# Kernel optimization log

Measured on AMD Instinct MI355X. Metric: run time of the kernel, lower is better.

## Reference

```python
import jax, jax.numpy as jnp
import numpy as np

D_MODEL = 1024
N_HEADS = 16
HEAD_DIM = D_MODEL // N_HEADS
SOFTMAX_SCALE = 1.0 / np.sqrt(HEAD_DIM).astype(np.float32)


def setup_inputs() -> dict:
    key = jax.random.key(0)
    k1, k2, k3, k4, k5 = jax.random.split(key, 5)
    B, S = 2, 2048
    bound_qkv = 1.0 / np.sqrt(D_MODEL)
    x = jax.random.normal(k1, (B, S, D_MODEL), dtype=jnp.float32)
    # torch nn.Linear stores weight as [out_features, in_features]
    Wqkv_w = jax.random.uniform(k2, (3 * D_MODEL, D_MODEL), jnp.float32, -bound_qkv, bound_qkv)
    Wqkv_b = jax.random.uniform(k3, (3 * D_MODEL,), jnp.float32, -bound_qkv, bound_qkv)
    Wout_w = jax.random.uniform(k4, (D_MODEL, D_MODEL), jnp.float32, -bound_qkv, bound_qkv)
    Wout_b = jax.random.uniform(k5, (D_MODEL,), jnp.float32, -bound_qkv, bound_qkv)
    return {"x": x, "Wqkv_w": Wqkv_w, "Wqkv_b": Wqkv_b, "Wout_w": Wout_w, "Wout_b": Wout_b}


def reference(x, Wqkv_w, Wqkv_b, Wout_w, Wout_b):
    B, S, D = x.shape
    # fused QKV projection
    qkv = jnp.einsum('bsd,ed->bse', x, Wqkv_w) + Wqkv_b  # [B, S, 3D]
    q, k, v = jnp.split(qkv, 3, axis=2)
    # b s (h d) -> b h s d
    q = q.reshape(B, S, N_HEADS, HEAD_DIM).transpose(0, 2, 1, 3)
    k = k.reshape(B, S, N_HEADS, HEAD_DIM).transpose(0, 2, 1, 3)
    v = v.reshape(B, S, N_HEADS, HEAD_DIM).transpose(0, 2, 1, 3)
    attn = jnp.einsum('bhsd,bhtd->bhst', q, k) * SOFTMAX_SCALE
    attn = jax.nn.softmax(attn, axis=-1)
    ctx = jnp.einsum('bhst,bhtd->bhsd', attn, v)
    ctx = ctx.transpose(0, 2, 1, 3).reshape(B, S, D)
    out = jnp.einsum('bsd,ed->bse', ctx, Wout_w) + Wout_b
    return out
```

## Files before the change

### kernel.cpp

```cpp
#include <hip/hip_runtime.h>
#include <hip/hip_bf16.h>

typedef __attribute__((ext_vector_type(8))) __bf16 bfrag;
typedef __attribute__((ext_vector_type(4))) float f32x4;
typedef __attribute__((ext_vector_type(16))) float f32x16;
typedef __attribute__((ext_vector_type(8))) unsigned short u16x8;
typedef __attribute__((ext_vector_type(4))) unsigned short u16x4;
typedef __attribute__((ext_vector_type(4))) unsigned int u32x4;

#define SEQ 2048
#define NH 16
#define HD 64
#define DMODEL 1024
#define MTOT 4096
#define QSCALE 0.18033688011112042f

static __device__ __forceinline__ unsigned short f2bf(float f) {
  unsigned int u = __builtin_bit_cast(unsigned int, f);
  u += 0x7FFFu + ((u >> 16) & 1u);
  return (unsigned short)(u >> 16);
}

static __device__ __forceinline__ unsigned cvt_pk_bf16(float lo, float hi) {
  unsigned r;
  asm("v_cvt_pk_bf16_f32 %0, %1, %2" : "=v"(r) : "v"(lo), "v"(hi));
  return r;
}

static __device__ __forceinline__ float rsum16(const f32x16 v) {
  float a0 = v[0] + v[1], a1 = v[2] + v[3], a2 = v[4] + v[5], a3 = v[6] + v[7];
  float a4 = v[8] + v[9], a5 = v[10] + v[11], a6 = v[12] + v[13], a7 = v[14] + v[15];
  float b0 = a0 + a1, b1 = a2 + a3, b2 = a4 + a5, b3 = a6 + a7;
  return (b0 + b1) + (b2 + b3);
}

#define XG 524288
#define WQG 393216
#define WOG 131072
__global__ __launch_bounds__(256) void cvt_all_kernel(const float* __restrict__ x,
                                                      const float* __restrict__ wq,
                                                      const float* __restrict__ wo,
                                                      unsigned short* __restrict__ out) {
  int i = blockIdx.x * 256 + threadIdx.x;
  if (i >= XG + WQG + WOG) return;
  const float4* p;
  if (i < XG) p = reinterpret_cast<const float4*>(x) + (size_t)i * 2;
  else if (i < XG + WQG) p = reinterpret_cast<const float4*>(wq) + (size_t)(i - XG) * 2;
  else p = reinterpret_cast<const float4*>(wo) + (size_t)(i - XG - WQG) * 2;
  float4 a = p[0], b = p[1];
  u16x8 o;
  o[0] = f2bf(a.x); o[1] = f2bf(a.y); o[2] = f2bf(a.z); o[3] = f2bf(a.w);
  o[4] = f2bf(b.x); o[5] = f2bf(b.y); o[6] = f2bf(b.z); o[7] = f2bf(b.w);
  *(reinterpret_cast<u16x8*>(out) + i) = o;
}

#define GLDS(gp, lp)                                                       \
  __builtin_amdgcn_global_load_lds(                                        \
      (const __attribute__((address_space(1))) void*)(gp),                 \
      (__attribute__((address_space(3))) void*)(lp), 16, 0, 0)

template <int EPI>
__global__ __launch_bounds__(256) void gemm_bt_kernel(
    const unsigned short* __restrict__ A, const unsigned short* __restrict__ B,
    const float* __restrict__ bias, unsigned short* __restrict__ q_out,
    unsigned short* __restrict__ k_out, unsigned short* __restrict__ v_out,
    float* __restrict__ f_out, int M, int N, int K) {
  __shared__ __align__(16) unsigned short As[3][4096];
  __shared__ __align__(16) unsigned short Bs[3][4096];
  const int t = threadIdx.x;
  const int l = t & 63, w = t >> 6;
  const int total = gridDim.x * gridDim.y;
  const int lid0 = blockIdx.y * gridDim.x + blockIdx.x;
  const int nl = (lid0 & 7) * (total >> 3) + (lid0 >> 3);
  const int m0 = (nl / gridDim.x) * 128, n0 = (nl % gridDim.x) * 128;
  const int wrow = (w >> 1) * 64, wcol = (w & 1) * 64;
  const int lrow = l & 15, lk = (l >> 4) * 8;
  const int srow = t >> 2;
  const int scol = ((t & 3) ^ (srow & 3)) * 8;
  f32x4 acc[4][4] = {};

#define GSTAGE(buf, K0)                                                     \
  do {                                                                      \
    GLDS(A + (size_t)(m0 + srow) * K + (K0) + scol, &As[buf][0] + t * 8);   \
    GLDS(A + (size_t)(m0 + srow + 64) * K + (K0) + scol,                    \
         &As[buf][0] + 2048 + t * 8);                                       \
    GLDS(B + (size_t)(n0 + srow) * K + (K0) + scol, &Bs[buf][0] + t * 8);   \
    GLDS(B + (size_t)(n0 + srow + 64) * K + (K0) + scol,                    \
         &Bs[buf][0] + 2048 + t * 8);                                       \
  } while (0)

  const int nsteps = K >> 5;
  GSTAGE(0, 0);
  GSTAGE(1, 32);
#pragma unroll 1
  for (int ks = 0; ks < nsteps; ++ks) {
    if (ks < nsteps - 1)
      asm volatile("s_waitcnt vmcnt(4)" ::: "memory");
    else
      asm volatile("s_waitcnt vmcnt(0)" ::: "memory");
    __builtin_amdgcn_s_barrier();
    __builtin_amdgcn_sched_barrier(0);
    if (ks + 2 < nsteps) GSTAGE((ks + 2) % 3, (ks + 2) * 32);
    const unsigned short* Ac = &As[ks % 3][0];
    const unsigned short* Bc = &Bs[ks % 3][0];
    bfrag af[4], bf[4];
#pragma unroll
    for (int mt = 0; mt < 4; ++mt) {
      int row = wrow + mt * 16 + lrow;
      af[mt] = *(const bfrag*)&Ac[row * 32 + (lk ^ ((row & 3) << 3))];
    }
#pragma unroll
    for (int nt = 0; nt < 4; ++nt) {
      int row = wcol + nt * 16 + lrow;
      bf[nt] = *(const bfrag*)&Bc[row * 32 + (lk ^ ((row & 3) << 3))];
    }
#pragma unroll
    for (int mt = 0; mt < 4; ++mt)
#pragma unroll
      for (int nt = 0; nt < 4; ++nt)
        acc[mt][nt] =
            __builtin_amdgcn_mfma_f32_16x16x32_bf16(af[mt], bf[nt], acc[mt][nt], 0, 0, 0);
  }
#undef GSTAGE
#pragma unroll
  for (int nt = 0; nt < 4; ++nt) {
    int gn = n0 + wcol + nt * 16 + lrow;
    float bv = bias[gn];
    if constexpr (EPI == 0) {
      int sel = gn >> 10;
      int e = gn & 1023;
      int h = e >> 6, d = e & 63;
#pragma unroll
      for (int mt = 0; mt < 4; ++mt) {
#pragma unroll
        for (int r = 0; r < 4; ++r) {
          int gm = m0 + wrow + mt * 16 + (l >> 4) * 4 + r;
          int b = gm >> 11, s = gm & 2047;
          float fv = acc[mt][nt][r] + bv;
          if (sel == 0)
            q_out[((size_t)(b * NH + h) * SEQ + s) * HD + d] = f2bf(fv * QSCALE);
          else if (sel == 1)
            k_out[((size_t)(b * NH + h) * SEQ + s) * HD + d] = f2bf(fv);
          else
            v_out[((size_t)(b * NH + h) * HD + d) * SEQ + s] = f2bf(fv);
        }
      }
    } else {
#pragma unroll
      for (int mt = 0; mt < 4; ++mt) {
#pragma unroll
        for (int r = 0; r < 4; ++r) {
          int gm = m0 + wrow + mt * 16 + (l >> 4) * 4 + r;
          f_out[(size_t)gm * N + gn] = acc[mt][nt][r] + bv;
        }
      }
    }
  }
}

__global__ __launch_bounds__(256, 2)
void attn_kernel(const unsigned short* __restrict__ Q,
                 const unsigned short* __restrict__ Km,
                 const unsigned short* __restrict__ Vt,
                 unsigned short* __restrict__ Ctx) {
  __shared__ __align__(16) unsigned short Ks[2][128 * 64];
  __shared__ __align__(16) unsigned short Vs[2][64 * 128];
  const int t = threadIdx.x;
  const int l = t & 63, w = t >> 6;
  const int q31 = l & 31, h = l >> 5;
  const int lid = blockIdx.y * gridDim.x + blockIdx.x;
  const int bh = (lid & 7) * 4 + ((lid >> 3) >> 4);
  const int q0 = ((lid >> 3) & 15) * 128 + w * 32;
  const unsigned short* qb = Q + (size_t)bh * SEQ * HD;
  const unsigned short* kb = Km + (size_t)bh * SEQ * HD;
  const unsigned short* vb = Vt + (size_t)bh * HD * SEQ;

  bfrag qf[4];
#pragma unroll
  for (int c = 0; c < 4; ++c)
    qf[c] = *(const bfrag*)&qb[(size_t)(q0 + q31) * HD + c * 16 + h * 8];

  f32x16 acc0 = {}, acc1 = {};
  float llocal = 0.f;

  const int skr = t >> 3;
  const int sks = ((t & 7) ^ (skr & 7)) * 8;
  const int svr = t >> 4;
  const int svs = ((t & 15) ^ svr) * 8;

#define STAGE(buf, T)                                                          \
  do {                                                                         \
    const int kv0_ = (T) * 128;                                                \
    _Pragma("unroll") for (int j = 0; j < 4; ++j)                              \
        GLDS(kb + (size_t)(kv0_ + 32 * j + skr) * HD + sks,                    \
             &Ks[buf][0] + j * 2048 + t * 8);                                  \
    _Pragma("unroll") for (int j = 0; j < 4; ++j)                              \
        GLDS(vb + (size_t)(16 * j + svr) * SEQ + kv0_ + svs,                   \
             &Vs[buf][0] + j * 2048 + t * 8);                                  \
  } while (0)

  STAGE(0, 0);
  __syncthreads();

  const int sw7 = q31 & 7, sw15 = q31 & 15;
  const int st0 = w & 3;

#define LOADK(kfv, stx)                                                        \
  _Pragma("unroll") for (int c = 0; c < 4; ++c)                                \
      kfv[c] = *(const bfrag*)&Kc[((stx) * 32 + q31) * 64 +                    \
                                  (((2 * c + h) ^ sw7) * 8)]

#define QK4(dst, kfv)                                                          \
  do {                                                                         \
    dst = (f32x16){};                                                          \
    __builtin_amdgcn_s_setprio(1);                                             \
    _Pragma("unroll") for (int c = 0; c < 4; ++c)                              \
        dst = __builtin_amdgcn_mfma_f32_32x32x16_bf16(kfv[c], qf[c], dst, 0, 0, 0); \
    __builtin_amdgcn_s_setprio(0);                                             \
  } while (0)

#define SOFTPV(stx, SV)                                                        \
  do {                                                                         \
    _Pragma("unroll") for (int r = 0; r < 16; ++r)                             \
        SV[r] = __builtin_amdgcn_exp2f(SV[r]);                                 \
    llocal += rsum16(SV);                                                      \
    _Pragma("unroll") for (int u = 0; u < 2; ++u) {                            \
      const int win = (stx) * 2 + u;                                           \
      const int bse = u * 8;                                                   \
      unsigned pk0 = cvt_pk_bf16(SV[bse + 0], SV[bse + 1]);                    \
      unsigned pk1 = cvt_pk_bf16(SV[bse + 2], SV[bse + 3]);                    \
      unsigned pk2 = cvt_pk_bf16(SV[bse + 4], SV[bse + 5]);                    \
      unsigned pk3 = cvt_pk_bf16(SV[bse + 6], SV[bse + 7]);                    \
      auto w02 = __builtin_amdgcn_permlane32_swap(pk0, pk2, false, false);     \
      auto w13 = __builtin_amdgcn_permlane32_swap(pk1, pk3, false, false);     \
      u32x4 bw = {(unsigned)w02[0], (unsigned)w13[0], (unsigned)w02[1],        \
                  (unsigned)w13[1]};                                           \
      bfrag pb = __builtin_bit_cast(bfrag, bw);                                \
      const int vchunk = ((win * 2 + h) ^ sw15) * 8;                           \
      bfrag vf0 = *(const bfrag*)&Vc[q31 * 128 + vchunk];                      \
      bfrag vf1 = *(const bfrag*)&Vc[(32 + q31) * 128 + vchunk];               \
      __builtin_amdgcn_s_setprio(1);                                           \
      acc0 = __builtin_amdgcn_mfma_f32_32x32x16_bf16(vf0, pb, acc0, 0, 0, 0);  \
      acc1 = __builtin_amdgcn_mfma_f32_32x32x16_bf16(vf1, pb, acc1, 0, 0, 0);  \
      __builtin_amdgcn_s_setprio(0);                                           \
    }                                                                          \
  } while (0)

#pragma unroll 1
  for (int t2 = 0; t2 < 16; ++t2) {
    const unsigned short* Kc = &Ks[t2 & 1][0];
    const unsigned short* Vc = &Vs[t2 & 1][0];
    bfrag kfa[4], kfb[4];
    f32x16 scur, snxt;
    LOADK(kfa, st0);
    QK4(scur, kfa);
    if (t2 < 15) STAGE((t2 + 1) & 1, t2 + 1);
#pragma unroll
    for (int j = 0; j < 4; ++j) {
      if (j < 3) {
        const int stn = (st0 + j + 1) & 3;
        LOADK(kfb, stn);
        QK4(snxt, kfb);
      }
      const int stc = (st0 + j) & 3;
      SOFTPV(stc, scur);
      scur = snxt;
    }
    __syncthreads();
  }
#undef STAGE
#undef LOADK
#undef QK4
#undef SOFTPV

  const int b = bh >> 4, head = bh & 15;
  float lsum = llocal + __shfl_xor(llocal, 32);
  const float inv = __builtin_amdgcn_rcpf(lsum);
  unsigned short* cp = Ctx + ((size_t)(b * SEQ + (q0 + q31)) * NH + head) * HD;
#pragma unroll
  for (int dt = 0; dt < 2; ++dt) {
    const f32x16 av = dt ? acc1 : acc0;
#pragma unroll
    for (int rq = 0; rq < 4; ++rq) {
      u16x4 o;
#pragma unroll
      for (int rr = 0; rr < 4; ++rr) o[rr] = f2bf(av[rq * 4 + rr] * inv);
      *(u16x4*)&cp[dt * 32 + rq * 8 + h * 4] = o;
    }
  }
}

extern "C" void kernel_launch(void* const* d_in, const int* in_sizes, int n_in,
                              void* d_out, int out_size, void* d_ws, size_t ws_size,
                              hipStream_t stream) {
  const float* x = (const float*)d_in[0];
  const float* wqkv = (const float*)d_in[1];
  const float* bqkv = (const float*)d_in[2];
  const float* wout = (const float*)d_in[3];
  const float* bout = (const float*)d_in[4];
  float* out = (float*)d_out;

  unsigned short* xb = (unsigned short*)d_ws;
  unsigned short* wqkvb = xb + (size_t)MTOT * DMODEL;
  unsigned short* woutb = wqkvb + (size_t)3 * DMODEL * DMODEL;
  unsigned short* qb = woutb + (size_t)DMODEL * DMODEL;
  unsigned short* kb = qb + (size_t)32 * SEQ * HD;
  unsigned short* vtb = kb + (size_t)32 * SEQ * HD;
  unsigned short* ctxb = vtb + (size_t)32 * SEQ * HD;

  cvt_all_kernel<<<(XG + WQG + WOG + 255) / 256, 256, 0, stream>>>(x, wqkv, wout, xb);
  gemm_bt_kernel<0><<<dim3(3 * DMODEL / 128, MTOT / 128), 256, 0, stream>>>(
      xb, wqkvb, bqkv, qb, kb, vtb, nullptr, MTOT, 3 * DMODEL, DMODEL);
  attn_kernel<<<dim3(SEQ / 128, 32), 256, 0, stream>>>(qb, kb, vtb, ctxb);
  gemm_bt_kernel<1><<<dim3(DMODEL / 128, MTOT / 128), 256, 0, stream>>>(
      ctxb, woutb, bout, nullptr, nullptr, nullptr, out, MTOT, DMODEL, DMODEL);
}
```

Baseline: 119.7 us.

## Switch GEMM to BK=64 double-buffered pipeline with 8-way XOR swizzle

The GEMM K-tile grows from 32 to 64, and the 3-stage LDS ring with fine-grained vmcnt waits becomes a 2-stage double buffer synchronised with __syncthreads. The LDS swizzle widens from 4-way to 8-way to match the 64-element rows. The aim is to halve the number of loop iterations and barriers and issue more MFMAs per step. In exchange, prefetch depth drops from two stages to one and the loop ends on a full-block barrier, which may expose more global-load latency.

```diff
diff --git a/kernel.cpp b/kernel.cpp
--- a/kernel.cpp
+++ b/kernel.cpp
@@ -65,8 +65,8 @@
     const float* __restrict__ bias, unsigned short* __restrict__ q_out,
     unsigned short* __restrict__ k_out, unsigned short* __restrict__ v_out,
     float* __restrict__ f_out, int M, int N, int K) {
-  __shared__ __align__(16) unsigned short As[3][4096];
-  __shared__ __align__(16) unsigned short Bs[3][4096];
+  __shared__ __align__(16) unsigned short As[2][8192];
+  __shared__ __align__(16) unsigned short Bs[2][8192];
   const int t = threadIdx.x;
   const int l = t & 63, w = t >> 6;
   const int total = gridDim.x * gridDim.y;
@@ -74,52 +74,53 @@
   const int nl = (lid0 & 7) * (total >> 3) + (lid0 >> 3);
   const int m0 = (nl / gridDim.x) * 128, n0 = (nl % gridDim.x) * 128;
   const int wrow = (w >> 1) * 64, wcol = (w & 1) * 64;
-  const int lrow = l & 15, lk = (l >> 4) * 8;
-  const int srow = t >> 2;
-  const int scol = ((t & 3) ^ (srow & 3)) * 8;
+  const int lrow = l & 15, hi = l >> 4;
+  const int srow = t >> 3;
+  const int scol = ((t & 7) ^ (srow & 7)) * 8;
   f32x4 acc[4][4] = {};
 
-#define GSTAGE(buf, K0)                                                     \
-  do {                                                                      \
-    GLDS(A + (size_t)(m0 + srow) * K + (K0) + scol, &As[buf][0] + t * 8);   \
-    GLDS(A + (size_t)(m0 + srow + 64) * K + (K0) + scol,                    \
-         &As[buf][0] + 2048 + t * 8);                                       \
-    GLDS(B + (size_t)(n0 + srow) * K + (K0) + scol, &Bs[buf][0] + t * 8);   \
-    GLDS(B + (size_t)(n0 + srow + 64) * K + (K0) + scol,                    \
-         &Bs[buf][0] + 2048 + t * 8);                                       \
+#define GSTAGE(buf, K0)                                                       \
+  do {                                                                        \
+    _Pragma("unroll") for (int j = 0; j < 4; ++j)                             \
+        GLDS(A + (size_t)(m0 + j * 32 + srow) * K + (K0) + scol,              \
+             &As[buf][0] + j * 2048 + t * 8);                                 \
+    _Pragma("unroll") for (int j = 0; j < 4; ++j)                             \
+        GLDS(B + (size_t)(n0 + j * 32 + srow) * K + (K0) + scol,              \
+             &Bs[buf][0] + j * 2048 + t * 8);                                 \
   } while (0)
 
-  const int nsteps = K >> 5;
+  const int nsteps = K >> 6;
   GSTAGE(0, 0);
-  GSTAGE(1, 32);
+  __syncthreads();
 #pragma unroll 1
-  for (int ks = 0; ks < nsteps; ++ks) {
-    if (ks < nsteps - 1)
-      asm volatile("s_waitcnt vmcnt(4)" ::: "memory");
-    else
-      asm volatile("s_waitcnt vmcnt(0)" ::: "memory");
-    __builtin_amdgcn_s_barrier();
-    __builtin_amdgcn_sched_barrier(0);
-    if (ks + 2 < nsteps) GSTAGE((ks + 2) % 3, (ks + 2) * 32);
-    const unsigned short* Ac = &As[ks % 3][0];
-    const unsigned short* Bc = &Bs[ks % 3][0];
-    bfrag af[4], bf[4];
+  for (int kt = 0; kt < nsteps; ++kt) {
+    if (kt < nsteps - 1) GSTAGE((kt + 1) & 1, (kt + 1) * 64);
+    const unsigned short* Ac = &As[kt & 1][0];
+    const unsigned short* Bc = &Bs[kt & 1][0];
+    bfrag af[4][2], bf[4][2];
 #pragma unroll
     for (int mt = 0; mt < 4; ++mt) {
-      int row = wrow + mt * 16 + lrow;
-      af[mt] = *(const bfrag*)&Ac[row * 32 + (lk ^ ((row & 3) << 3))];
+      const int row = wrow + mt * 16 + lrow;
+#pragma unroll
+      for (int ks = 0; ks < 2; ++ks)
+        af[mt][ks] = *(const bfrag*)&Ac[row * 64 + (((hi + ks * 4) ^ (row & 7)) * 8)];
     }
 #pragma unroll
     for (int nt = 0; nt < 4; ++nt) {
-      int row = wcol + nt * 16 + lrow;
-      bf[nt] = *(const bfrag*)&Bc[row * 32 + (lk ^ ((row & 3) << 3))];
+      const int row = wcol + nt * 16 + lrow;
+#pragma unroll
+      for (int ks = 0; ks < 2; ++ks)
+        bf[nt][ks] = *(const bfrag*)&Bc[row * 64 + (((hi + ks * 4) ^ (row & 7)) * 8)];
     }
 #pragma unroll
     for (int mt = 0; mt < 4; ++mt)
 #pragma unroll
       for (int nt = 0; nt < 4; ++nt)
-        acc[mt][nt] =
-            __builtin_amdgcn_mfma_f32_16x16x32_bf16(af[mt], bf[nt], acc[mt][nt], 0, 0, 0);
+#pragma unroll
+        for (int ks = 0; ks < 2; ++ks)
+          acc[mt][nt] = __builtin_amdgcn_mfma_f32_16x16x32_bf16(af[mt][ks], bf[nt][ks],
+                                                                acc[mt][nt], 0, 0, 0);
+    __syncthreads();
   }
 #undef GSTAGE
 #pragma unroll
@@ -134,7 +135,7 @@
       for (int mt = 0; mt < 4; ++mt) {
 #pragma unroll
         for (int r = 0; r < 4; ++r) {
-          int gm = m0 + wrow + mt * 16 + (l >> 4) * 4 + r;
+          int gm = m0 + wrow + mt * 16 + hi * 4 + r;
           int b = gm >> 11, s = gm & 2047;
           float fv = acc[mt][nt][r] + bv;
           if (sel == 0)
@@ -150,7 +151,7 @@
       for (int mt = 0; mt < 4; ++mt) {
 #pragma unroll
         for (int r = 0; r < 4; ++r) {
-          int gm = m0 + wrow + mt * 16 + (l >> 4) * 4 + r;
+          int gm = m0 + wrow + mt * 16 + hi * 4 + r;
           f_out[(size_t)gm * N + gn] = acc[mt][nt][r] + bv;
         }
       }
```

After: 127.5 us. 1.06x slower.
